# Kernel tuning notes

Measured on AMD Instinct MI355X. Metric: run time of the kernel, lower is better.

## Reference

```python
import jax, jax.numpy as jnp
import numpy as np

B, N, C_IN, C_OUT, K = 8, 1024, 64, 64, 4


def setup_inputs() -> dict:
    key = jax.random.key(0)
    k1, k2, k3 = jax.random.split(key, 3)
    x = jax.random.normal(k1, (B, N, C_IN), dtype=jnp.float32)
    # scaled-Laplacian-like matrix; 1/sqrt(N) scaling keeps Chebyshev recurrence stable
    L = jax.random.normal(k2, (B, N, N), dtype=jnp.float32) * (1.0 / np.sqrt(N))
    theta = jax.random.normal(k3, (K, C_IN, C_OUT), dtype=jnp.float32) * np.sqrt(2.0 / C_IN)
    return {"x": x, "L": L, "theta": theta}


def reference(x, L, theta):
    # Chebyshev recurrence applied directly to feature vectors:
    #   z0 = x, z1 = L x, z_k = 2 L z_{k-1} - z_{k-2}
    # out = sum_k z_k @ theta[k]  -- same math as materializing T_k(L),
    # since T_k(L) @ x obeys the same 3-term recurrence.
    k_orders = theta.shape[0]
    z_prev = x                      # [B,N,C]
    out = jnp.matmul(z_prev, theta[0])
    if k_orders > 1:
        z_curr = jnp.matmul(L, x)   # [B,N,C]
        out = out + jnp.matmul(z_curr, theta[1])
        for k in range(2, k_orders):
            z_next = 2.0 * jnp.matmul(L, z_curr) - z_prev
            out = out + jnp.matmul(z_next, theta[k])
            z_prev, z_curr = z_curr, z_next
    return out
```

## Files before the change

kernel.cpp:

```cpp
#include <hip/hip_runtime.h>
#include <cstdint>
#include <cstddef>


typedef __bf16 bf16;
typedef bf16 bf16x8 __attribute__((ext_vector_type(8)));
typedef float f32x4 __attribute__((ext_vector_type(4)));

#define MFMA_BF16(a, b, c) __builtin_amdgcn_mfma_f32_16x16x32_bf16((a), (b), (c), 0, 0, 0)
#define WAITV(n) asm volatile("s_waitcnt vmcnt(" #n ")" ::: "memory")

__device__ __forceinline__ void dma16(const void* g, void* l) {
    __builtin_amdgcn_global_load_lds(
        (const __attribute__((address_space(1))) unsigned int*)g,
        (__attribute__((address_space(3))) unsigned int*)l, 16, 0, 0);
}

__global__ __launch_bounds__(256) void prep_kernel(const float* __restrict__ x,
                                                   const float* __restrict__ theta,
                                                   bf16* __restrict__ xT,
                                                   bf16* __restrict__ xb,
                                                   bf16* __restrict__ thT)
{
    __shared__ bf16 tile[64][72];
    const int bid = blockIdx.x;
    const int t = threadIdx.x;
    const int r = t >> 2;
    const int c0 = (t & 3) << 4;

    const float* src;
    bf16* dstT;
    int dst_ld;
    const bool isx = bid < 128;
    int b = 0, n0 = 0;
    if (isx) {
        b = bid >> 4; n0 = (bid & 15) << 6;
        src = x + (size_t)(b * 1024 + n0) * 64;
        dstT = xT + (size_t)b * 64 * 1024 + n0;
        dst_ld = 1024;
    } else {
        const int k = bid - 128;
        src = theta + (size_t)k * 4096;
        dstT = thT + (size_t)k * 4096;
        dst_ld = 64;
    }

    bf16x8 row0, row1;
#pragma unroll
    for (int j = 0; j < 16; j += 4) {
        f32x4 v = *reinterpret_cast<const f32x4*>(src + r * 64 + c0 + j);
#pragma unroll
        for (int i = 0; i < 4; ++i) {
            bf16 q = (bf16)v[i];
            tile[r][c0 + j + i] = q;
            if (j + i < 8) row0[j + i] = q; else row1[j + i - 8] = q;
        }
    }
    if (isx) {
        bf16* xr = xb + (size_t)(b * 1024 + n0 + r) * 64 + c0;
        *reinterpret_cast<bf16x8*>(xr) = row0;
        *reinterpret_cast<bf16x8*>(xr + 8) = row1;
    }
    __syncthreads();
    bf16x8 o0, o1;
#pragma unroll
    for (int j = 0; j < 8; ++j) { o0[j] = tile[c0 + j][r]; o1[j] = tile[c0 + 8 + j][r]; }
    *reinterpret_cast<bf16x8*>(dstT + (size_t)r * dst_ld + c0) = o0;
    *reinterpret_cast<bf16x8*>(dstT + (size_t)r * dst_ld + c0 + 8) = o1;
}

template <int STAGE>
__global__ __launch_bounds__(256) void stage_kernel(
    const float* __restrict__ Lmat,
    const bf16* __restrict__ xb,
    const bf16* __restrict__ zinT,
    const bf16* __restrict__ zprevT,
    const bf16* __restrict__ thT,
    bf16* __restrict__ zoutT,
    float* __restrict__ out)
{
    constexpr int D = 5, T = 16, KS = 64, LSTG = 12288;
    __shared__ __align__(16) unsigned char smem[D * LSTG + 16 * 72 * 2];

    const int bid = blockIdx.x;
    const int b  = bid >> 6;
    const int m0 = (bid & 63) << 4;
    const int t  = threadIdx.x;
    const int w  = t >> 6;
    const int l  = t & 63;
    const int l15 = l & 15;
    const int lg  = l >> 4;
    const int c0  = w << 4;

    const float* Lrb = Lmat + ((size_t)(b * 1024 + m0)) * 1024;
    const bf16*  zb  = zinT + (size_t)b * 64 * 1024;

    const int Lrow = t >> 4, Lslot = t & 15;
    const float* Lsrc = Lrb + (size_t)Lrow * 1024 + (Lslot ^ (Lrow & 7)) * 4;
    const int Zg0 = (w << 7) + l, Zg1 = Zg0 + 64;
    const int Zch0 = Zg0 >> 3, Zch1 = Zg1 >> 3;
    const bf16* Zsrc0 = zb + (size_t)Zch0 * 1024 + ((Zg0 & 7) ^ (Zch0 & 7)) * 8;
    const bf16* Zsrc1 = zb + (size_t)Zch1 * 1024 + ((Zg1 & 7) ^ (Zch1 & 7)) * 8;

    auto issue = [&](int k0, unsigned char* bufb) {
        dma16(Lsrc + k0, bufb + (w << 10));
        dma16(Zsrc0 + k0, bufb + 4096 + (w << 11));
        dma16(Zsrc1 + k0, bufb + 4096 + (w << 11) + 1024);
    };

    f32x4 acc = {0.f, 0.f, 0.f, 0.f};

    auto computeStep = [&](const unsigned char* bufb) {
        const float* Ll = (const float*)bufb;
        const bf16*  Zl = (const bf16*)(bufb + 4096);
        const int chan = c0 + l15;
        const int sA = chan & 7;
        bf16x8 a0 = *(const bf16x8*)(Zl + (((chan << 3) + (lg ^ sA)) << 3));
        bf16x8 a1 = *(const bf16x8*)(Zl + (((chan << 3) + ((4 + lg) ^ sA)) << 3));
        const int sB = l15 & 7;
        const float* Lr = Ll + (l15 << 6);
        f32x4 u0 = *(const f32x4*)(Lr + ((((lg << 1) | 0) ^ sB) << 2));
        f32x4 u1 = *(const f32x4*)(Lr + ((((lg << 1) | 1) ^ sB) << 2));
        f32x4 v0 = *(const f32x4*)(Lr + (((8 + ((lg << 1) | 0)) ^ sB) << 2));
        f32x4 v1 = *(const f32x4*)(Lr + (((8 + ((lg << 1) | 1)) ^ sB) << 2));
        bf16x8 b0, b1;
#pragma unroll
        for (int j = 0; j < 4; ++j) {
            b0[j] = (bf16)u0[j]; b0[4 + j] = (bf16)u1[j];
            b1[j] = (bf16)v0[j]; b1[4 + j] = (bf16)v1[j];
        }
        acc = MFMA_BF16(a0, b0, acc);
        acc = MFMA_BF16(a1, b1, acc);
    };

#pragma unroll
    for (int s = 0; s < D - 1; ++s)
        issue(s * KS, smem + s * LSTG);

#pragma unroll
    for (int tt = 0; tt < T; ++tt) {
        const int rem = (T - 1 - tt) < (D - 2) ? (T - 1 - tt) : (D - 2);
        if (rem >= 3)      WAITV(9);
        else if (rem == 2) WAITV(6);
        else if (rem == 1) WAITV(3);
        else               WAITV(0);
        __builtin_amdgcn_sched_barrier(0);
        __builtin_amdgcn_s_barrier();
        __builtin_amdgcn_sched_barrier(0);
        computeStep(smem + (tt % D) * LSTG);
        if (tt + D - 1 < T)
            issue((tt + D - 1) * KS, smem + ((tt + D - 1) % D) * LSTG);
    }

    bf16 (*zbuf)[72] = (bf16(*)[72])(smem + D * LSTG);
    const int cr = c0 + (lg << 2);
    const float alpha = (STAGE == 1) ? 1.0f : 2.0f;
    float zv[4];
#pragma unroll
    for (int r = 0; r < 4; ++r) {
        float zp = 0.f;
        if constexpr (STAGE >= 2)
            zp = (float)zprevT[(size_t)(b * 64 + cr + r) * 1024 + m0 + l15];
        zv[r] = alpha * acc[r] - zp;
    }
    if constexpr (STAGE <= 2) {
#pragma unroll
        for (int r = 0; r < 4; ++r)
            zoutT[(size_t)(b * 64 + cr + r) * 1024 + m0 + l15] = (bf16)zv[r];
    }
#pragma unroll
    for (int r = 0; r < 4; ++r)
        zbuf[l15][cr + r] = (bf16)zv[r];
    __syncthreads();

    const int o = (w << 4) + l15;
    f32x4 oacc;
    if constexpr (STAGE == 1) {
        oacc = (f32x4){0.f, 0.f, 0.f, 0.f};
#pragma unroll
        for (int ck = 0; ck < 2; ++ck) {
            bf16x8 ax = *reinterpret_cast<const bf16x8*>(
                xb + (size_t)(b * 1024 + m0 + l15) * 64 + ck * 32 + lg * 8);
            bf16x8 bt = *reinterpret_cast<const bf16x8*>(
                thT + (size_t)o * 64 + ck * 32 + lg * 8);
            oacc = MFMA_BF16(ax, bt, oacc);
        }
    } else {
#pragma unroll
        for (int r = 0; r < 4; ++r)
            oacc[r] = out[(size_t)(b * 1024 + m0 + lg * 4 + r) * 64 + o];
    }
    constexpr int KTH = (STAGE == 1) ? 1 : STAGE;
#pragma unroll
    for (int ck = 0; ck < 2; ++ck) {
        bf16x8 az = *reinterpret_cast<const bf16x8*>(&zbuf[l15][ck * 32 + lg * 8]);
        bf16x8 bt = *reinterpret_cast<const bf16x8*>(
            thT + (size_t)(KTH * 64 + o) * 64 + ck * 32 + lg * 8);
        oacc = MFMA_BF16(az, bt, oacc);
    }
#pragma unroll
    for (int r = 0; r < 4; ++r)
        out[(size_t)(b * 1024 + m0 + lg * 4 + r) * 64 + o] = oacc[r];
}

extern "C" void kernel_launch(void* const* d_in, const int* in_sizes, int n_in,
                              void* d_out, int out_size, void* d_ws, size_t ws_size,
                              hipStream_t stream)
{
    const float* x  = (const float*)d_in[0];
    const float* L  = (const float*)d_in[1];
    const float* th = (const float*)d_in[2];
    float* out = (float*)d_out;

    bf16* xT  = (bf16*)d_ws;
    bf16* xb  = xT  + (size_t)8 * 64 * 1024;
    bf16* z1T = xb  + (size_t)8 * 64 * 1024;
    bf16* z2T = z1T + (size_t)8 * 64 * 1024;
    bf16* thT = z2T + (size_t)8 * 64 * 1024;

    prep_kernel<<<dim3(132), dim3(256), 0, stream>>>(x, th, xT, xb, thT);
    stage_kernel<1><<<dim3(512), dim3(256), 0, stream>>>(L, xb, xT, xT, thT, z1T, out);
    stage_kernel<2><<<dim3(512), dim3(256), 0, stream>>>(L, xb, z1T, xT, thT, z2T, out);
    stage_kernel<3><<<dim3(512), dim3(256), 0, stream>>>(L, xb, z2T, z1T, thT, nullptr, out);
}
```

Baseline: 112.2 us.

## Fuse prep and three Chebyshev stages into one cooperative kernel with grid syncs

Replaces four separate kernel launches with a single cooperative kernel that runs the prep transpose, then the three stages, separated by grid-wide syncs. The output accumulator now stays in registers across stages instead of being written to and re-read from global memory each stage. This removes launch gaps and the round trips of the output through memory. In exchange it adds grid.sync barriers, and it requires all 512 blocks to be co-resident, which the cooperative launch enforces. That residency depends on the LDS footprint allowing two blocks per CU.

```diff
diff --git a/kernel.cpp b/kernel.cpp
--- a/kernel.cpp
+++ b/kernel.cpp
@@ -1,6 +1,9 @@
 #include <hip/hip_runtime.h>
+#include <hip/hip_cooperative_groups.h>
 #include <cstdint>
 #include <cstddef>
+
+namespace cg = cooperative_groups;
 
 
 typedef __bf16 bf16;
@@ -16,76 +19,21 @@
         (__attribute__((address_space(3))) unsigned int*)l, 16, 0, 0);
 }
 
-__global__ __launch_bounds__(256) void prep_kernel(const float* __restrict__ x,
-                                                   const float* __restrict__ theta,
-                                                   bf16* __restrict__ xT,
-                                                   bf16* __restrict__ xb,
-                                                   bf16* __restrict__ thT)
-{
-    __shared__ bf16 tile[64][72];
-    const int bid = blockIdx.x;
-    const int t = threadIdx.x;
-    const int r = t >> 2;
-    const int c0 = (t & 3) << 4;
-
-    const float* src;
-    bf16* dstT;
-    int dst_ld;
-    const bool isx = bid < 128;
-    int b = 0, n0 = 0;
-    if (isx) {
-        b = bid >> 4; n0 = (bid & 15) << 6;
-        src = x + (size_t)(b * 1024 + n0) * 64;
-        dstT = xT + (size_t)b * 64 * 1024 + n0;
-        dst_ld = 1024;
-    } else {
-        const int k = bid - 128;
-        src = theta + (size_t)k * 4096;
-        dstT = thT + (size_t)k * 4096;
-        dst_ld = 64;
-    }
-
-    bf16x8 row0, row1;
-#pragma unroll
-    for (int j = 0; j < 16; j += 4) {
-        f32x4 v = *reinterpret_cast<const f32x4*>(src + r * 64 + c0 + j);
-#pragma unroll
-        for (int i = 0; i < 4; ++i) {
-            bf16 q = (bf16)v[i];
-            tile[r][c0 + j + i] = q;
-            if (j + i < 8) row0[j + i] = q; else row1[j + i - 8] = q;
-        }
-    }
-    if (isx) {
-        bf16* xr = xb + (size_t)(b * 1024 + n0 + r) * 64 + c0;
-        *reinterpret_cast<bf16x8*>(xr) = row0;
-        *reinterpret_cast<bf16x8*>(xr + 8) = row1;
-    }
-    __syncthreads();
-    bf16x8 o0, o1;
-#pragma unroll
-    for (int j = 0; j < 8; ++j) { o0[j] = tile[c0 + j][r]; o1[j] = tile[c0 + 8 + j][r]; }
-    *reinterpret_cast<bf16x8*>(dstT + (size_t)r * dst_ld + c0) = o0;
-    *reinterpret_cast<bf16x8*>(dstT + (size_t)r * dst_ld + c0 + 8) = o1;
-}
+constexpr int D_ = 5, T_ = 16, KS_ = 64, LSTG_ = 12288;
+constexpr int SMEM_BYTES = D_ * LSTG_ + 16 * 72 * 2;
 
 template <int STAGE>
-__global__ __launch_bounds__(256) void stage_kernel(
+__device__ __forceinline__ void stage_body(
+    int b, int m0, int t,
     const float* __restrict__ Lmat,
     const bf16* __restrict__ xb,
     const bf16* __restrict__ zinT,
     const bf16* __restrict__ zprevT,
     const bf16* __restrict__ thT,
     bf16* __restrict__ zoutT,
-    float* __restrict__ out)
+    unsigned char* smem,
+    f32x4& oacc)
 {
-    constexpr int D = 5, T = 16, KS = 64, LSTG = 12288;
-    __shared__ __align__(16) unsigned char smem[D * LSTG + 16 * 72 * 2];
-
-    const int bid = blockIdx.x;
-    const int b  = bid >> 6;
-    const int m0 = (bid & 63) << 4;
-    const int t  = threadIdx.x;
     const int w  = t >> 6;
     const int l  = t & 63;
     const int l15 = l & 15;
@@ -133,13 +81,15 @@
         acc = MFMA_BF16(a1, b1, acc);
     };
 
-#pragma unroll
-    for (int s = 0; s < D - 1; ++s)
-        issue(s * KS, smem + s * LSTG);
-
-#pragma unroll
-    for (int tt = 0; tt < T; ++tt) {
-        const int rem = (T - 1 - tt) < (D - 2) ? (T - 1 - tt) : (D - 2);
+    WAITV(0);
+    __builtin_amdgcn_sched_barrier(0);
+#pragma unroll
+    for (int s = 0; s < D_ - 1; ++s)
+        issue(s * KS_, smem + s * LSTG_);
+
+#pragma unroll
+    for (int tt = 0; tt < T_; ++tt) {
+        const int rem = (T_ - 1 - tt) < (D_ - 2) ? (T_ - 1 - tt) : (D_ - 2);
         if (rem >= 3)      WAITV(9);
         else if (rem == 2) WAITV(6);
         else if (rem == 1) WAITV(3);
@@ -147,12 +97,12 @@
         __builtin_amdgcn_sched_barrier(0);
         __builtin_amdgcn_s_barrier();
         __builtin_amdgcn_sched_barrier(0);
-        computeStep(smem + (tt % D) * LSTG);
-        if (tt + D - 1 < T)
-            issue((tt + D - 1) * KS, smem + ((tt + D - 1) % D) * LSTG);
-    }
-
-    bf16 (*zbuf)[72] = (bf16(*)[72])(smem + D * LSTG);
+        computeStep(smem + (tt % D_) * LSTG_);
+        if (tt + D_ - 1 < T_)
+            issue((tt + D_ - 1) * KS_, smem + ((tt + D_ - 1) % D_) * LSTG_);
+    }
+
+    bf16 (*zbuf)[72] = (bf16(*)[72])(smem + D_ * LSTG_);
     const int cr = c0 + (lg << 2);
     const float alpha = (STAGE == 1) ? 1.0f : 2.0f;
     float zv[4];
@@ -174,9 +124,7 @@
     __syncthreads();
 
     const int o = (w << 4) + l15;
-    f32x4 oacc;
     if constexpr (STAGE == 1) {
-        oacc = (f32x4){0.f, 0.f, 0.f, 0.f};
 #pragma unroll
         for (int ck = 0; ck < 2; ++ck) {
             bf16x8 ax = *reinterpret_cast<const bf16x8*>(
@@ -185,10 +133,6 @@
                 thT + (size_t)o * 64 + ck * 32 + lg * 8);
             oacc = MFMA_BF16(ax, bt, oacc);
         }
-    } else {
-#pragma unroll
-        for (int r = 0; r < 4; ++r)
-            oacc[r] = out[(size_t)(b * 1024 + m0 + lg * 4 + r) * 64 + o];
     }
     constexpr int KTH = (STAGE == 1) ? 1 : STAGE;
 #pragma unroll
@@ -198,6 +142,81 @@
             thT + (size_t)(KTH * 64 + o) * 64 + ck * 32 + lg * 8);
         oacc = MFMA_BF16(az, bt, oacc);
     }
+    __syncthreads();
+}
+
+__global__ __launch_bounds__(256) void fused_kernel(
+    const float* __restrict__ x, const float* __restrict__ Lmat,
+    const float* __restrict__ theta,
+    bf16* __restrict__ xT, bf16* __restrict__ xb, bf16* __restrict__ thT,
+    bf16* __restrict__ z1T, bf16* __restrict__ z2T,
+    float* __restrict__ out)
+{
+    __shared__ __align__(16) unsigned char smem[SMEM_BYTES];
+    cg::grid_group grid = cg::this_grid();
+    const int bid = blockIdx.x;
+    const int t = threadIdx.x;
+
+    if (bid < 132) {
+        bf16 (*tile)[72] = reinterpret_cast<bf16(*)[72]>(smem);
+        const int r = t >> 2;
+        const int c0 = (t & 3) << 4;
+        const float* src;
+        bf16* dstT;
+        int dst_ld;
+        const bool isx = bid < 128;
+        int b = 0, n0 = 0;
+        if (isx) {
+            b = bid >> 4; n0 = (bid & 15) << 6;
+            src = x + (size_t)(b * 1024 + n0) * 64;
+            dstT = xT + (size_t)b * 64 * 1024 + n0;
+            dst_ld = 1024;
+        } else {
+            const int k = bid - 128;
+            src = theta + (size_t)k * 4096;
+            dstT = thT + (size_t)k * 4096;
+            dst_ld = 64;
+        }
+        bf16x8 row0, row1;
+#pragma unroll
+        for (int j = 0; j < 16; j += 4) {
+            f32x4 v = *reinterpret_cast<const f32x4*>(src + r * 64 + c0 + j);
+#pragma unroll
+            for (int i = 0; i < 4; ++i) {
+                bf16 q = (bf16)v[i];
+                tile[r][c0 + j + i] = q;
+                if (j + i < 8) row0[j + i] = q; else row1[j + i - 8] = q;
+            }
+        }
+        if (isx) {
+            bf16* xr = xb + (size_t)(b * 1024 + n0 + r) * 64 + c0;
+            *reinterpret_cast<bf16x8*>(xr) = row0;
+            *reinterpret_cast<bf16x8*>(xr + 8) = row1;
+        }
+        __syncthreads();
+        bf16x8 o0, o1;
+#pragma unroll
+        for (int j = 0; j < 8; ++j) { o0[j] = tile[c0 + j][r]; o1[j] = tile[c0 + 8 + j][r]; }
+        *reinterpret_cast<bf16x8*>(dstT + (size_t)r * dst_ld + c0) = o0;
+        *reinterpret_cast<bf16x8*>(dstT + (size_t)r * dst_ld + c0 + 8) = o1;
+    }
+    __threadfence();
+    grid.sync();
+
+    const int b  = bid >> 6;
+    const int m0 = (bid & 63) << 4;
+    f32x4 oacc = {0.f, 0.f, 0.f, 0.f};
+
+    stage_body<1>(b, m0, t, Lmat, xb, xT, nullptr, thT, z1T, smem, oacc);
+    __threadfence();
+    grid.sync();
+    stage_body<2>(b, m0, t, Lmat, xb, z1T, xT, thT, z2T, smem, oacc);
+    __threadfence();
+    grid.sync();
+    stage_body<3>(b, m0, t, Lmat, xb, z2T, z1T, thT, nullptr, smem, oacc);
+
+    const int w = t >> 6, l = t & 63, l15 = l & 15, lg = l >> 4;
+    const int o = (w << 4) + l15;
 #pragma unroll
     for (int r = 0; r < 4; ++r)
         out[(size_t)(b * 1024 + m0 + lg * 4 + r) * 64 + o] = oacc[r];
@@ -218,8 +237,9 @@
     bf16* z2T = z1T + (size_t)8 * 64 * 1024;
     bf16* thT = z2T + (size_t)8 * 64 * 1024;
 
-    prep_kernel<<<dim3(132), dim3(256), 0, stream>>>(x, th, xT, xb, thT);
-    stage_kernel<1><<<dim3(512), dim3(256), 0, stream>>>(L, xb, xT, xT, thT, z1T, out);
-    stage_kernel<2><<<dim3(512), dim3(256), 0, stream>>>(L, xb, z1T, xT, thT, z2T, out);
-    stage_kernel<3><<<dim3(512), dim3(256), 0, stream>>>(L, xb, z2T, z1T, thT, nullptr, out);
-}
+    void* args[] = { (void*)&x, (void*)&L, (void*)&th,
+                     (void*)&xT, (void*)&xb, (void*)&thT,
+                     (void*)&z1T, (void*)&z2T, (void*)&out };
+    hipLaunchCooperativeKernel((void*)fused_kernel, dim3(512), dim3(256),
+                               args, 0, stream);
+}
```

After: 419.4 us. +273.9%, slower.

## Pre-convert L to bf16 once in prep kernel and stream bf16 L in stages

Applied to the files above, without the earlier changes.

The prep kernel gains extra blocks that convert the whole fp32 L matrix to a bf16 workspace copy. The three stage kernels then DMA bf16 L tiles, which halves the L bytes loaded per stage and shrinks the LDS stage size. It also removes the per-step fp32-to-bf16 conversion inside the inner loop, replacing it with direct bf16x8 LDS reads. The cost is an extra full pass that reads 32MB and writes 16MB before the first stage, so total L traffic stays roughly the same and the gain depends on the stages being limited by latency or conversion rather than bandwidth.

```diff
diff --git a/kernel.cpp b/kernel.cpp
--- a/kernel.cpp
+++ b/kernel.cpp
@@ -4,6 +4,7 @@
 
 
 typedef __bf16 bf16;
+typedef bf16 bf16x4 __attribute__((ext_vector_type(4)));
 typedef bf16 bf16x8 __attribute__((ext_vector_type(8)));
 typedef float f32x4 __attribute__((ext_vector_type(4)));
 
@@ -18,16 +19,31 @@
 
 __global__ __launch_bounds__(256) void prep_kernel(const float* __restrict__ x,
                                                    const float* __restrict__ theta,
+                                                   const float* __restrict__ Lmat,
                                                    bf16* __restrict__ xT,
                                                    bf16* __restrict__ xb,
-                                                   bf16* __restrict__ thT)
+                                                   bf16* __restrict__ thT,
+                                                   bf16* __restrict__ Lb)
 {
-    __shared__ bf16 tile[64][72];
     const int bid = blockIdx.x;
     const int t = threadIdx.x;
+
+    if (bid >= 132) {
+        constexpr int CHUNKS = (8 * 1024 * 1024) / 4;
+        const int stride = (1156 - 132) * 256;
+        for (int idx = (bid - 132) * 256 + t; idx < CHUNKS; idx += stride) {
+            f32x4 v = ((const f32x4*)Lmat)[idx];
+            bf16x4 q;
+#pragma unroll
+            for (int i = 0; i < 4; ++i) q[i] = (bf16)v[i];
+            ((bf16x4*)Lb)[idx] = q;
+        }
+        return;
+    }
+
+    __shared__ bf16 tile[64][72];
     const int r = t >> 2;
     const int c0 = (t & 3) << 4;
-
     const float* src;
     bf16* dstT;
     int dst_ld;
@@ -71,7 +87,7 @@
 
 template <int STAGE>
 __global__ __launch_bounds__(256) void stage_kernel(
-    const float* __restrict__ Lmat,
+    const bf16* __restrict__ Lb,
     const bf16* __restrict__ xb,
     const bf16* __restrict__ zinT,
     const bf16* __restrict__ zprevT,
@@ -79,7 +95,7 @@
     bf16* __restrict__ zoutT,
     float* __restrict__ out)
 {
-    constexpr int D = 5, T = 16, KS = 64, LSTG = 12288;
+    constexpr int D = 5, T = 16, KS = 64, LSTG = 10240;
     __shared__ __align__(16) unsigned char smem[D * LSTG + 16 * 72 * 2];
 
     const int bid = blockIdx.x;
@@ -92,43 +108,36 @@
     const int lg  = l >> 4;
     const int c0  = w << 4;
 
-    const float* Lrb = Lmat + ((size_t)(b * 1024 + m0)) * 1024;
-    const bf16*  zb  = zinT + (size_t)b * 64 * 1024;
-
-    const int Lrow = t >> 4, Lslot = t & 15;
-    const float* Lsrc = Lrb + (size_t)Lrow * 1024 + (Lslot ^ (Lrow & 7)) * 4;
+    const bf16* Lrb = Lb + ((size_t)(b * 1024 + m0)) * 1024;
+    const bf16* zb  = zinT + (size_t)b * 64 * 1024;
+
+    const int Lg = (w << 5) + (l & 31);
+    const int Lrow = Lg >> 3, Lslot = Lg & 7;
+    const bf16* Lsrc = Lrb + (size_t)Lrow * 1024 + (Lslot ^ (Lrow & 7)) * 8;
     const int Zg0 = (w << 7) + l, Zg1 = Zg0 + 64;
     const int Zch0 = Zg0 >> 3, Zch1 = Zg1 >> 3;
     const bf16* Zsrc0 = zb + (size_t)Zch0 * 1024 + ((Zg0 & 7) ^ (Zch0 & 7)) * 8;
     const bf16* Zsrc1 = zb + (size_t)Zch1 * 1024 + ((Zg1 & 7) ^ (Zch1 & 7)) * 8;
 
     auto issue = [&](int k0, unsigned char* bufb) {
-        dma16(Lsrc + k0, bufb + (w << 10));
-        dma16(Zsrc0 + k0, bufb + 4096 + (w << 11));
-        dma16(Zsrc1 + k0, bufb + 4096 + (w << 11) + 1024);
+        dma16(Zsrc0 + k0, bufb + 2048 + (w << 11));
+        dma16(Zsrc1 + k0, bufb + 2048 + (w << 11) + 1024);
+        if (l < 32)
+            dma16(Lsrc + k0, bufb + (w << 9));
     };
 
     f32x4 acc = {0.f, 0.f, 0.f, 0.f};
 
     auto computeStep = [&](const unsigned char* bufb) {
-        const float* Ll = (const float*)bufb;
-        const bf16*  Zl = (const bf16*)(bufb + 4096);
+        const bf16* Ll = (const bf16*)bufb;
+        const bf16* Zl = (const bf16*)(bufb + 2048);
         const int chan = c0 + l15;
         const int sA = chan & 7;
         bf16x8 a0 = *(const bf16x8*)(Zl + (((chan << 3) + (lg ^ sA)) << 3));
         bf16x8 a1 = *(const bf16x8*)(Zl + (((chan << 3) + ((4 + lg) ^ sA)) << 3));
         const int sB = l15 & 7;
-        const float* Lr = Ll + (l15 << 6);
-        f32x4 u0 = *(const f32x4*)(Lr + ((((lg << 1) | 0) ^ sB) << 2));
-        f32x4 u1 = *(const f32x4*)(Lr + ((((lg << 1) | 1) ^ sB) << 2));
-        f32x4 v0 = *(const f32x4*)(Lr + (((8 + ((lg << 1) | 0)) ^ sB) << 2));
-        f32x4 v1 = *(const f32x4*)(Lr + (((8 + ((lg << 1) | 1)) ^ sB) << 2));
-        bf16x8 b0, b1;
-#pragma unroll
-        for (int j = 0; j < 4; ++j) {
-            b0[j] = (bf16)u0[j]; b0[4 + j] = (bf16)u1[j];
-            b1[j] = (bf16)v0[j]; b1[4 + j] = (bf16)v1[j];
-        }
+        bf16x8 b0 = *(const bf16x8*)(Ll + (((l15 << 3) + (lg ^ sB)) << 3));
+        bf16x8 b1 = *(const bf16x8*)(Ll + (((l15 << 3) + ((4 + lg) ^ sB)) << 3));
         acc = MFMA_BF16(a0, b0, acc);
         acc = MFMA_BF16(a1, b1, acc);
     };
@@ -217,9 +226,10 @@
     bf16* z1T = xb  + (size_t)8 * 64 * 1024;
     bf16* z2T = z1T + (size_t)8 * 64 * 1024;
     bf16* thT = z2T + (size_t)8 * 64 * 1024;
-
-    prep_kernel<<<dim3(132), dim3(256), 0, stream>>>(x, th, xT, xb, thT);
-    stage_kernel<1><<<dim3(512), dim3(256), 0, stream>>>(L, xb, xT, xT, thT, z1T, out);
-    stage_kernel<2><<<dim3(512), dim3(256), 0, stream>>>(L, xb, z1T, xT, thT, z2T, out);
-    stage_kernel<3><<<dim3(512), dim3(256), 0, stream>>>(L, xb, z2T, z1T, thT, nullptr, out);
-}
+    bf16* Lb  = thT + (size_t)4 * 64 * 64;
+
+    prep_kernel<<<dim3(1156), dim3(256), 0, stream>>>(x, th, L, xT, xb, thT, Lb);
+    stage_kernel<1><<<dim3(512), dim3(256), 0, stream>>>(Lb, xb, xT, nullptr, thT, z1T, out);
+    stage_kernel<2><<<dim3(512), dim3(256), 0, stream>>>(Lb, xb, z1T, xT, thT, z2T, out);
+    stage_kernel<3><<<dim3(512), dim3(256), 0, stream>>>(Lb, xb, z2T, z1T, thT, nullptr, out);
+}
```

After: 101.7 us. -9.3%, faster.
